# Performance work log

Measured on AMD Instinct MI355X. Metric: run time of the kernel, lower is better.

The kernel has to match this reference:

```python
import jax, jax.numpy as jnp
import numpy as np

B = 65536  # batch of independent scalar inputs
NQ = 6     # qubits -> state shape (B, 2,2,2,2,2,2); qubit 0 = leftmost axis


def _sel(q, bit, controls):
    ix = [slice(None)] * (NQ + 1)
    for cq in controls:
        ix[cq + 1] = 1
    ix[q + 1] = bit
    return tuple(ix)


def _ry(state, q, theta, controls=()):
    """(Controlled-)RY on qubit q. theta: scalar or (B,) array."""
    half = jnp.asarray(theta) * 0.5
    c, s = jnp.cos(half), jnp.sin(half)
    i0, i1 = _sel(q, 0, controls), _sel(q, 1, controls)
    a0, a1 = state[i0], state[i1]
    if c.ndim:  # batched angle -> broadcast over remaining qubit axes
        bs = (c.shape[0],) + (1,) * (a0.ndim - 1)
        c, s = c.reshape(bs), s.reshape(bs)
    state = state.at[i0].set(c * a0 - s * a1)
    return state.at[i1].set(s * a0 + c * a1)


def _y(state, q, controls=()):
    """(Controlled-)Pauli-Y on qubit q: |0>->i|1>, |1>->-i|0>."""
    i0, i1 = _sel(q, 0, controls), _sel(q, 1, controls)
    a0, a1 = state[i0], state[i1]
    state = state.at[i0].set(-1j * a1)
    return state.at[i1].set(1j * a0)


def _circuit(x, p):
    n = x.shape[0]
    st = jnp.zeros((n,) + (2,) * NQ, jnp.complex64)
    st = st.at[(slice(None),) + (0,) * NQ].set(1.0)
    # -- data encoding block 1 --
    st = _ry(st, 0, x * 3.0); st = _ry(st, 1, x * 9.0); st = _ry(st, 2, x)
    # -- variational layer on qubits 0..2 --
    st = _ry(st, 0, p[0]); st = _ry(st, 1, p[1]); st = _ry(st, 2, p[2])
    # -- controlled rotations onto qubits 3,4,5 --
    st = _ry(st, 3, p[3], (2,)); st = _ry(st, 3, p[4], (1,)); st = _ry(st, 3, p[5], (0,)); st = _ry(st, 3, p[6])
    st = _ry(st, 4, p[7], (2,)); st = _ry(st, 4, p[8], (1,)); st = _ry(st, 4, p[9], (0,)); st = _ry(st, 4, p[10])
    st = _ry(st, 5, p[11], (2,)); st = _ry(st, 5, p[12], (1,)); st = _ry(st, 5, p[13], (0,)); st = _ry(st, 5, p[14])
    st = _ry(st, 3, 0.5); st = _ry(st, 4, 0.5); st = _ry(st, 5, 0.5)
    # -- entangling block among qubits 3,4,5 --
    st = _ry(st, 4, p[15], (3,)); st = _ry(st, 5, p[16], (3,))
    st = _ry(st, 3, p[17], (4,)); st = _ry(st, 5, p[18], (4,))
    st = _ry(st, 3, p[19], (5,)); st = _ry(st, 4, p[20], (5,))
    st = _ry(st, 3, p[21]); st = _ry(st, 4, p[22]); st = _ry(st, 5, p[23])
    # -- triply-controlled Y back onto qubits 0..2 --
    st = _y(st, 0, (3, 4, 5)); st = _y(st, 1, (3, 4, 5)); st = _y(st, 2, (3, 4, 5))
    # -- data encoding block 2 --
    st = _ry(st, 0, x * 7.0); st = _ry(st, 1, x * 17.0); st = _ry(st, 2, x)
    st = _ry(st, 0, p[24]); st = _ry(st, 1, p[25]); st = _ry(st, 2, p[26])
    st = _ry(st, 0, -0.5); st = _ry(st, 1, -0.5); st = _ry(st, 2, -0.5)
    # -- entangling block among qubits 0,1,2 --
    st = _ry(st, 1, p[27], (0,)); st = _ry(st, 2, p[28], (0,))
    st = _ry(st, 0, p[29], (1,)); st = _ry(st, 2, p[30], (1,))
    st = _ry(st, 0, p[31], (2,)); st = _ry(st, 1, p[32], (2,))
    st = _ry(st, 0, p[33]); st = _ry(st, 1, p[34]); st = _ry(st, 2, p[35])
    # marginal probabilities of qubits (0,1,2) being 000 / 111
    p000 = jnp.sum(jnp.abs(st[:, 0, 0, 0]) ** 2, axis=(1, 2, 3))
    p111 = jnp.sum(jnp.abs(st[:, 1, 1, 1]) ** 2, axis=(1, 2, 3))
    return (p111 - p000) * 2.0


def setup_inputs() -> dict:
    key = jax.random.key(0)
    k1, k2 = jax.random.split(key)
    inputs = jax.random.uniform(k1, (B,), dtype=jnp.float32)
    params = jax.random.uniform(k2, (36,), dtype=jnp.float32) * (2.0 * np.pi)
    return {"inputs": inputs, "params": params}


def reference(inputs, params):
    return _circuit(inputs, params)
```

## Files before the change

kernel.cpp:

```cpp
#include <hip/hip_runtime.h>


template <int TB, int CB>
__device__ __forceinline__ void ry_r(float* st, float c, float s) {
#pragma unroll
    for (int r = 0; r < 8; ++r) {
        if (r & TB) continue;
        if (CB && !(r & CB)) continue;
        float a0 = st[r], a1 = st[r + TB];
        st[r]      = fmaf(c, a0, -(s * a1));
        st[r + TB] = fmaf(s, a0, c * a1);
    }
}

template <int TB, int LCM>
__device__ __forceinline__ void gate_r(float* st, int lane, float c, float s) {
    if (LCM) {
        bool act = (lane & LCM) == LCM;
        c = act ? c : 1.0f;
        s = act ? s : 0.0f;
    }
    ry_r<TB, 0>(st, c, s);
}

template <int XM>
__device__ __forceinline__ void ry_x(float* st, float c, float ssgn) {
#pragma unroll
    for (int r = 0; r < 8; ++r) {
        float pr = __shfl_xor(st[r], XM);
        st[r] = fmaf(c, st[r], ssgn * pr);
    }
}

template <int XM, int LCM>
__device__ __forceinline__ void gate_x(float* st, int lane, float c, float s) {
    float ssgn = (lane & XM) ? s : -s;
    if (LCM) {
        bool act = (lane & LCM) == LCM;
        c = act ? c : 1.0f;
        ssgn = act ? ssgn : 0.0f;
    }
    ry_x<XM>(st, c, ssgn);
}

__global__ __launch_bounds__(256) void pnn_kernel(const float* __restrict__ x,
                                                  const float* __restrict__ p,
                                                  float* __restrict__ out,
                                                  int n) {
    int gtid = blockIdx.x * blockDim.x + threadIdx.x;
    int e = gtid >> 3;
    int lane = gtid & 7;
    if (e >= n) return;
    float xv = x[e];

    float st[8];
#pragma unroll
    for (int r = 0; r < 8; ++r) st[r] = 0.0f;
    if (lane == 0) st[0] = 1.0f;

    float c, s;
    auto cs = [&](float th) { __sincosf(th * 0.5f, &s, &c); };

    cs(xv * 3.0f); gate_x<4, 0>(st, lane, c, s);
    cs(xv * 9.0f); gate_x<2, 0>(st, lane, c, s);
    cs(xv);        gate_x<1, 0>(st, lane, c, s);
    cs(p[0]); gate_x<4, 0>(st, lane, c, s);
    cs(p[1]); gate_x<2, 0>(st, lane, c, s);
    cs(p[2]); gate_x<1, 0>(st, lane, c, s);
    cs(p[3]); gate_r<4, 1>(st, lane, c, s);
    cs(p[4]); gate_r<4, 2>(st, lane, c, s);
    cs(p[5]); gate_r<4, 4>(st, lane, c, s);
    cs(p[6]); gate_r<4, 0>(st, lane, c, s);
    cs(p[7]);  gate_r<2, 1>(st, lane, c, s);
    cs(p[8]);  gate_r<2, 2>(st, lane, c, s);
    cs(p[9]);  gate_r<2, 4>(st, lane, c, s);
    cs(p[10]); gate_r<2, 0>(st, lane, c, s);
    cs(p[11]); gate_r<1, 1>(st, lane, c, s);
    cs(p[12]); gate_r<1, 2>(st, lane, c, s);
    cs(p[13]); gate_r<1, 4>(st, lane, c, s);
    cs(p[14]); gate_r<1, 0>(st, lane, c, s);
    cs(0.5f);
    ry_r<4, 0>(st, c, s); ry_r<2, 0>(st, c, s); ry_r<1, 0>(st, c, s);
    cs(p[15]); ry_r<2, 4>(st, c, s);
    cs(p[16]); ry_r<1, 4>(st, c, s);
    cs(p[17]); ry_r<4, 2>(st, c, s);
    cs(p[18]); ry_r<1, 2>(st, c, s);
    cs(p[19]); ry_r<4, 1>(st, c, s);
    cs(p[20]); ry_r<2, 1>(st, c, s);
    cs(p[21]); ry_r<4, 0>(st, c, s);
    cs(p[22]); ry_r<2, 0>(st, c, s);
    cs(p[23]); ry_r<1, 0>(st, c, s);

    {
        float ysign = (__popc(lane) & 1) ? -1.0f : 1.0f;
        float pr = __shfl_xor(st[7], 7);
        st[7] = ysign * pr;
    }

    cs(xv * 7.0f);  gate_x<4, 0>(st, lane, c, s);
    cs(xv * 17.0f); gate_x<2, 0>(st, lane, c, s);
    cs(xv);         gate_x<1, 0>(st, lane, c, s);
    cs(p[24]); gate_x<4, 0>(st, lane, c, s);
    cs(p[25]); gate_x<2, 0>(st, lane, c, s);
    cs(p[26]); gate_x<1, 0>(st, lane, c, s);
    cs(-0.5f);
    gate_x<4, 0>(st, lane, c, s);
    gate_x<2, 0>(st, lane, c, s);
    gate_x<1, 0>(st, lane, c, s);
    cs(p[27]); gate_x<2, 4>(st, lane, c, s);
    cs(p[28]); gate_x<1, 4>(st, lane, c, s);
    cs(p[29]); gate_x<4, 2>(st, lane, c, s);
    cs(p[30]); gate_x<1, 2>(st, lane, c, s);
    cs(p[31]); gate_x<4, 1>(st, lane, c, s);
    cs(p[32]); gate_x<2, 1>(st, lane, c, s);
    cs(p[33]); gate_x<4, 0>(st, lane, c, s);
    cs(p[34]); gate_x<2, 0>(st, lane, c, s);
    cs(p[35]); gate_x<1, 0>(st, lane, c, s);

    float psum = 0.0f;
#pragma unroll
    for (int r = 0; r < 8; ++r) psum = fmaf(st[r], st[r], psum);
    float other = __shfl_xor(psum, 7);
    if (lane == 0) out[e] = (other - psum) * 2.0f;
}

extern "C" void kernel_launch(void* const* d_in, const int* in_sizes, int n_in,
                              void* d_out, int out_size, void* d_ws, size_t ws_size,
                              hipStream_t stream) {
    const float* x = (const float*)d_in[0];
    const float* p = (const float*)d_in[1];
    float* out = (float*)d_out;
    int n = in_sizes[0];
    long long threads = (long long)n * 8;
    int block = 256;
    int grid = (int)((threads + block - 1) / block);
    pnn_kernel<<<grid, block, 0, stream>>>(x, p, out, n);
}
```

Before: 69.05 us.

## Fuse same-qubit RY rotations and replace shfl_xor with DPP/swizzle lane permutes

Consecutive RY rotations on the same qubit are merged by adding their angles. This removes nine gates along with their sincos evaluations and state updates. Cross-lane exchanges previously done with __shfl_xor, which goes through ds_bpermute, now use DPP quad_perm, row_half_mirror and ds_swizzle. Those are cheaper intra-row permutes. The trade-off is a tiny rounding difference from the summed angles, plus a dependence on the 8-lane group layout matching the DPP patterns.

```diff
diff --git a/kernel.cpp b/kernel.cpp
--- a/kernel.cpp
+++ b/kernel.cpp
@@ -1,5 +1,20 @@
 #include <hip/hip_runtime.h>
 
+
+template <int XM>
+__device__ __forceinline__ float lane_perm(float v) {
+    int i = __float_as_int(v);
+    int r;
+    if constexpr (XM == 1)
+        r = __builtin_amdgcn_update_dpp(i, i, 0xB1, 0xF, 0xF, 0);
+    else if constexpr (XM == 2)
+        r = __builtin_amdgcn_update_dpp(i, i, 0x4E, 0xF, 0xF, 0);
+    else if constexpr (XM == 4)
+        r = __builtin_amdgcn_ds_swizzle(i, 0x101F);
+    else
+        r = __builtin_amdgcn_update_dpp(i, i, 0x141, 0xF, 0xF, 0);
+    return __int_as_float(r);
+}
 
 template <int TB, int CB>
 __device__ __forceinline__ void ry_r(float* st, float c, float s) {
@@ -23,15 +38,6 @@
     ry_r<TB, 0>(st, c, s);
 }
 
-template <int XM>
-__device__ __forceinline__ void ry_x(float* st, float c, float ssgn) {
-#pragma unroll
-    for (int r = 0; r < 8; ++r) {
-        float pr = __shfl_xor(st[r], XM);
-        st[r] = fmaf(c, st[r], ssgn * pr);
-    }
-}
-
 template <int XM, int LCM>
 __device__ __forceinline__ void gate_x(float* st, int lane, float c, float s) {
     float ssgn = (lane & XM) ? s : -s;
@@ -40,7 +46,11 @@
         c = act ? c : 1.0f;
         ssgn = act ? ssgn : 0.0f;
     }
-    ry_x<XM>(st, c, ssgn);
+#pragma unroll
+    for (int r = 0; r < 8; ++r) {
+        float pr = lane_perm<XM>(st[r]);
+        st[r] = fmaf(c, st[r], ssgn * pr);
+    }
 }
 
 __global__ __launch_bounds__(256) void pnn_kernel(const float* __restrict__ x,
@@ -61,26 +71,21 @@
     float c, s;
     auto cs = [&](float th) { __sincosf(th * 0.5f, &s, &c); };
 
-    cs(xv * 3.0f); gate_x<4, 0>(st, lane, c, s);
-    cs(xv * 9.0f); gate_x<2, 0>(st, lane, c, s);
-    cs(xv);        gate_x<1, 0>(st, lane, c, s);
-    cs(p[0]); gate_x<4, 0>(st, lane, c, s);
-    cs(p[1]); gate_x<2, 0>(st, lane, c, s);
-    cs(p[2]); gate_x<1, 0>(st, lane, c, s);
-    cs(p[3]); gate_r<4, 1>(st, lane, c, s);
-    cs(p[4]); gate_r<4, 2>(st, lane, c, s);
-    cs(p[5]); gate_r<4, 4>(st, lane, c, s);
-    cs(p[6]); gate_r<4, 0>(st, lane, c, s);
-    cs(p[7]);  gate_r<2, 1>(st, lane, c, s);
-    cs(p[8]);  gate_r<2, 2>(st, lane, c, s);
-    cs(p[9]);  gate_r<2, 4>(st, lane, c, s);
-    cs(p[10]); gate_r<2, 0>(st, lane, c, s);
-    cs(p[11]); gate_r<1, 1>(st, lane, c, s);
-    cs(p[12]); gate_r<1, 2>(st, lane, c, s);
-    cs(p[13]); gate_r<1, 4>(st, lane, c, s);
-    cs(p[14]); gate_r<1, 0>(st, lane, c, s);
-    cs(0.5f);
-    ry_r<4, 0>(st, c, s); ry_r<2, 0>(st, c, s); ry_r<1, 0>(st, c, s);
+    cs(fmaf(xv, 3.0f, p[0])); gate_x<4, 0>(st, lane, c, s);
+    cs(fmaf(xv, 9.0f, p[1])); gate_x<2, 0>(st, lane, c, s);
+    cs(xv + p[2]);            gate_x<1, 0>(st, lane, c, s);
+    cs(p[3]);        gate_r<4, 1>(st, lane, c, s);
+    cs(p[4]);        gate_r<4, 2>(st, lane, c, s);
+    cs(p[5]);        gate_r<4, 4>(st, lane, c, s);
+    cs(p[6] + 0.5f); ry_r<4, 0>(st, c, s);
+    cs(p[7]);         gate_r<2, 1>(st, lane, c, s);
+    cs(p[8]);         gate_r<2, 2>(st, lane, c, s);
+    cs(p[9]);         gate_r<2, 4>(st, lane, c, s);
+    cs(p[10] + 0.5f); ry_r<2, 0>(st, c, s);
+    cs(p[11]);        gate_r<1, 1>(st, lane, c, s);
+    cs(p[12]);        gate_r<1, 2>(st, lane, c, s);
+    cs(p[13]);        gate_r<1, 4>(st, lane, c, s);
+    cs(p[14] + 0.5f); ry_r<1, 0>(st, c, s);
     cs(p[15]); ry_r<2, 4>(st, c, s);
     cs(p[16]); ry_r<1, 4>(st, c, s);
     cs(p[17]); ry_r<4, 2>(st, c, s);
@@ -93,20 +98,12 @@
 
     {
         float ysign = (__popc(lane) & 1) ? -1.0f : 1.0f;
-        float pr = __shfl_xor(st[7], 7);
-        st[7] = ysign * pr;
+        st[7] = ysign * lane_perm<7>(st[7]);
     }
 
-    cs(xv * 7.0f);  gate_x<4, 0>(st, lane, c, s);
-    cs(xv * 17.0f); gate_x<2, 0>(st, lane, c, s);
-    cs(xv);         gate_x<1, 0>(st, lane, c, s);
-    cs(p[24]); gate_x<4, 0>(st, lane, c, s);
-    cs(p[25]); gate_x<2, 0>(st, lane, c, s);
-    cs(p[26]); gate_x<1, 0>(st, lane, c, s);
-    cs(-0.5f);
-    gate_x<4, 0>(st, lane, c, s);
-    gate_x<2, 0>(st, lane, c, s);
-    gate_x<1, 0>(st, lane, c, s);
+    cs(fmaf(xv, 7.0f, p[24]) - 0.5f);  gate_x<4, 0>(st, lane, c, s);
+    cs(fmaf(xv, 17.0f, p[25]) - 0.5f); gate_x<2, 0>(st, lane, c, s);
+    cs(xv + p[26] - 0.5f);             gate_x<1, 0>(st, lane, c, s);
     cs(p[27]); gate_x<2, 4>(st, lane, c, s);
     cs(p[28]); gate_x<1, 4>(st, lane, c, s);
     cs(p[29]); gate_x<4, 2>(st, lane, c, s);
@@ -120,7 +117,7 @@
     float psum = 0.0f;
 #pragma unroll
     for (int r = 0; r < 8; ++r) psum = fmaf(st[r], st[r], psum);
-    float other = __shfl_xor(psum, 7);
+    float other = lane_perm<7>(psum);
     if (lane == 0) out[e] = (other - psum) * 2.0f;
 }
 
```

Result: faster. 65.06 us (-5.8%).
